# Kernel tuning notes

Measured on AMD Instinct MI355X. Metric: run time of the kernel, lower is better.

## Reference

```python
import jax, jax.numpy as jnp
import numpy as np

B, NA, DIN, H, DOUT = 8192, 32, 8, 64, 8  # B must be divisible by NA (final reshape)


def setup_inputs() -> dict:
    key = jax.random.key(0)
    ks = jax.random.split(key, 9)
    rn = lambda k, shp, s=1.0: jax.random.normal(k, shp, dtype=jnp.float32) * s
    return {
        "x": rn(ks[0], (B, NA, DIN)),
        "laplacian": jax.random.uniform(ks[1], (B, NA, 1), dtype=jnp.float32),
        "W_in": rn(ks[2], (H, DIN), 1.0 / np.sqrt(DIN)),
        "b_in": rn(ks[3], (H,), 0.01),
        "Aq": rn(ks[4], (H, H)),   # torch.randn init in original
        "Ak": rn(ks[5], (H, H)),
        "Av": rn(ks[6], (H, H)),
        "W_out": rn(ks[7], (DOUT, H), 1.0 / np.sqrt(H)),
        "b_out": rn(ks[8], (DOUT,), 0.01),
    }


def reference(x, laplacian, W_in, b_in, Aq, Ak, Av, W_out, b_out):
    silu = jax.nn.silu
    # mlp_in = SiLU(Linear); kron(laplacian, ones(1,1,H)) == broadcast of (B,na,1) mask
    h = silu(x @ W_in.T + b_in) * laplacian            # (B, na, H)
    # Q/K/V: weight @ h^T with swish; attention is over the HIDDEN axis (H x H scores)
    Q = silu(jnp.einsum('ij,bnj->bin', Aq, h))         # (B, H, na)
    K = silu(jnp.einsum('ij,bnj->bni', Ak, h))         # (B, na, H)
    V = silu(jnp.einsum('ij,bnj->bin', Av, h))         # (B, H, na)
    A = jax.nn.softmax(jnp.einsum('bin,bnj->bij', Q, K), axis=2)  # (B, H, H), softmax dim=2
    attn = silu(jnp.einsum('bij,bjn->bni', A, V))      # (B, na, H)
    # mlp_out = SiLU(Linear), masked again, mean over nodes, reshape (B/na, na, O)
    y = silu(attn @ W_out.T + b_out) * laplacian       # (B, na, O)
    return y.mean(axis=1).reshape(-1, NA, DOUT)        # (B/NA, NA, O)
```

## Files before the change

### kernel.cpp

```cpp
#include <hip/hip_runtime.h>

#define NB   8192
#define NA   32
#define DIN  8
#define HID  64
#define DOUT 8

typedef float     v4f __attribute__((ext_vector_type(4)));
typedef _Float16  v4h __attribute__((ext_vector_type(4)));

__device__ __forceinline__ float silu_f(float x) {
    return __fdividef(x, 1.0f + __expf(-x));
}

__device__ __forceinline__ v4h cvt4(v4f a) {
    v4h r;
    r[0] = (_Float16)a[0]; r[1] = (_Float16)a[1];
    r[2] = (_Float16)a[2]; r[3] = (_Float16)a[3];
    return r;
}

__device__ __forceinline__ v4h silu_cvt4(v4f a) {
    v4f s;
    s[0] = silu_f(a[0]); s[1] = silu_f(a[1]);
    s[2] = silu_f(a[2]); s[3] = silu_f(a[3]);
    return cvt4(s);
}

#define MFMA16(A, B, C) __builtin_amdgcn_mfma_f32_16x16x16f16((A), (B), (C), 0, 0, 0)

__global__ __launch_bounds__(256, 5) void attn_mfma_kernel(
    const float* __restrict__ x,
    const float* __restrict__ lap,
    const float* __restrict__ W_in,
    const float* __restrict__ b_in,
    const float* __restrict__ Aq,
    const float* __restrict__ Ak,
    const float* __restrict__ Av,
    const float* __restrict__ W_out,
    const float* __restrict__ b_out,
    float* __restrict__ out)
{
    __shared__ _Float16 wlds[3][16][64][4];
    __shared__ _Float16 hlds[4][4][64][4];

    const int t  = threadIdx.x;
    const int l  = t & 63;
    const int w  = t >> 6;
    const int lm = l & 15;
    const int lg = l >> 4;

    {
        const float* mats[3] = {Aq, Ak, Av};
        #pragma unroll
        for (int m = 0; m < 3; ++m) {
            #pragma unroll
            for (int f = 0; f < 4; ++f) {
                const int fid = w * 4 + f;
                const int it = fid >> 2, ks = fid & 3;
                v4f v = *(const v4f*)(mats[m] + (lm + 16 * it) * 64 + 16 * ks + 4 * lg);
                *(v4h*)&wlds[m][fid][l][0] = cvt4(v);
            }
        }
    }

    v4h zh = {};
    v4f zf = {};
    v4h winf[4];
    #pragma unroll
    for (int jt = 0; jt < 4; ++jt)
        winf[jt] = (lg < 2) ? cvt4(*(const v4f*)(W_in + (lm + 16 * jt) * 8 + 4 * lg)) : zh;
    v4h woutf[4];
    #pragma unroll
    for (int ks = 0; ks < 4; ++ks)
        woutf[ks] = (lm < 8) ? cvt4(*(const v4f*)(W_out + lm * 64 + 16 * ks + 4 * lg)) : zh;
    float binf[4];
    #pragma unroll
    for (int jt = 0; jt < 4; ++jt) binf[jt] = b_in[lm + 16 * jt];
    const float boutf = (lm < 8) ? b_out[lm] : 0.0f;

    __syncthreads();

    const int b = blockIdx.x * 4 + w;

    v4f lapv[2];
    lapv[0] = *(const v4f*)(lap + b * 32 + 4 * lg);
    lapv[1] = *(const v4f*)(lap + b * 32 + 16 + 4 * lg);

    v4h xf[2];
    #pragma unroll
    for (int nt = 0; nt < 2; ++nt)
        xf[nt] = (lg < 2) ? cvt4(*(const v4f*)(x + b * 256 + (lm + 16 * nt) * 8 + 4 * lg)) : zh;

    const int pr = l ^ lg;
    v4h hf[2][4];
    #pragma unroll
    for (int nt = 0; nt < 2; ++nt) {
        #pragma unroll
        for (int jt = 0; jt < 4; ++jt) {
            v4f hc = MFMA16(xf[nt], winf[jt], zf);
            #pragma unroll
            for (int r = 0; r < 4; ++r) {
                float hv = silu_f(hc[r] + binf[jt]) * lapv[nt][r];
                const int lr   = (4 * lg + r) | ((lm >> 2) << 4);
                const int phys = lr ^ (lm >> 2);
                hlds[w][jt][phys][lm & 3] = (_Float16)hv;
            }
        }
        __builtin_amdgcn_s_waitcnt(0);
        #pragma unroll
        for (int ks = 0; ks < 4; ++ks)
            hf[nt][ks] = *(v4h*)&hlds[w][ks][pr][0];
        __builtin_amdgcn_s_waitcnt(0);
    }

    v4h qf[2][4];
    {
        v4f acc[2][4] = {};
        #pragma unroll
        for (int it = 0; it < 4; ++it)
            #pragma unroll
            for (int ks = 0; ks < 4; ++ks) {
                v4h bw = *(v4h*)&wlds[0][it * 4 + ks][l][0];
                #pragma unroll
                for (int nt = 0; nt < 2; ++nt)
                    acc[nt][it] = MFMA16(hf[nt][ks], bw, acc[nt][it]);
            }
        #pragma unroll
        for (int nt = 0; nt < 2; ++nt)
            #pragma unroll
            for (int it = 0; it < 4; ++it) qf[nt][it] = silu_cvt4(acc[nt][it]);
    }
    v4h kf[2][4];
    {
        v4f acc[2][4] = {};
        #pragma unroll
        for (int it = 0; it < 4; ++it)
            #pragma unroll
            for (int ks = 0; ks < 4; ++ks) {
                v4h bw = *(v4h*)&wlds[1][it * 4 + ks][l][0];
                #pragma unroll
                for (int nt = 0; nt < 2; ++nt)
                    acc[nt][it] = MFMA16(hf[nt][ks], bw, acc[nt][it]);
            }
        #pragma unroll
        for (int nt = 0; nt < 2; ++nt)
            #pragma unroll
            for (int it = 0; it < 4; ++it) kf[nt][it] = silu_cvt4(acc[nt][it]);
    }
    v4h vf[4][2];
    {
        v4f acc[4][2] = {};
        #pragma unroll
        for (int it = 0; it < 4; ++it)
            #pragma unroll
            for (int ks = 0; ks < 4; ++ks) {
                v4h aw = *(v4h*)&wlds[2][it * 4 + ks][l][0];
                #pragma unroll
                for (int nt = 0; nt < 2; ++nt)
                    acc[it][nt] = MFMA16(aw, hf[nt][ks], acc[it][nt]);
            }
        #pragma unroll
        for (int it = 0; it < 4; ++it)
            #pragma unroll
            for (int nt = 0; nt < 2; ++nt) vf[it][nt] = silu_cvt4(acc[it][nt]);
    }

    v4f st[4][4] = {};
    #pragma unroll
    for (int jt = 0; jt < 4; ++jt)
        #pragma unroll
        for (int it = 0; it < 4; ++it)
            #pragma unroll
            for (int ns = 0; ns < 2; ++ns)
                st[jt][it] = MFMA16(kf[ns][jt], qf[ns][it], st[jt][it]);

    v4h pf[4][4];
    #pragma unroll
    for (int it = 0; it < 4; ++it) {
        float mx = st[0][it][0];
        #pragma unroll
        for (int jt = 0; jt < 4; ++jt)
            #pragma unroll
            for (int r = 0; r < 4; ++r) mx = fmaxf(mx, st[jt][it][r]);
        mx = fmaxf(mx, __shfl_xor(mx, 16, 64));
        mx = fmaxf(mx, __shfl_xor(mx, 32, 64));
        float sum = 0.0f;
        #pragma unroll
        for (int jt = 0; jt < 4; ++jt)
            #pragma unroll
            for (int r = 0; r < 4; ++r) {
                float e = __expf(st[jt][it][r] - mx);
                st[jt][it][r] = e;
                sum += e;
            }
        sum += __shfl_xor(sum, 16, 64);
        sum += __shfl_xor(sum, 32, 64);
        const float inv = __fdividef(1.0f, sum);
        #pragma unroll
        for (int jt = 0; jt < 4; ++jt) {
            v4f p = st[jt][it] * inv;
            pf[it][jt] = cvt4(p);
        }
    }

    v4f pv[4][2] = {};
    #pragma unroll
    for (int it = 0; it < 4; ++it)
        #pragma unroll
        for (int js = 0; js < 4; ++js)
            #pragma unroll
            for (int nt = 0; nt < 2; ++nt)
                pv[it][nt] = MFMA16(pf[it][js], vf[js][nt], pv[it][nt]);

    v4f ya[2] = {};
    #pragma unroll
    for (int nt = 0; nt < 2; ++nt)
        #pragma unroll
        for (int is = 0; is < 4; ++is)
            ya[nt] = MFMA16(silu_cvt4(pv[is][nt]), woutf[is], ya[nt]);

    float acc = 0.0f;
    #pragma unroll
    for (int nt = 0; nt < 2; ++nt)
        #pragma unroll
        for (int r = 0; r < 4; ++r)
            acc += silu_f(ya[nt][r] + boutf) * lapv[nt][r];
    acc += __shfl_xor(acc, 16, 64);
    acc += __shfl_xor(acc, 32, 64);
    if (l < 8) out[b * DOUT + l] = acc * (1.0f / NA);
}

extern "C" void kernel_launch(void* const* d_in, const int* in_sizes, int n_in,
                              void* d_out, int out_size, void* d_ws, size_t ws_size,
                              hipStream_t stream) {
    const float* x     = (const float*)d_in[0];
    const float* lap   = (const float*)d_in[1];
    const float* W_in  = (const float*)d_in[2];
    const float* b_in  = (const float*)d_in[3];
    const float* Aq    = (const float*)d_in[4];
    const float* Ak    = (const float*)d_in[5];
    const float* Av    = (const float*)d_in[6];
    const float* W_out = (const float*)d_in[7];
    const float* b_out = (const float*)d_in[8];
    attn_mfma_kernel<<<2048, 256, 0, stream>>>(x, lap, W_in, b_in, Aq, Ak, Av,
                                               W_out, b_out, (float*)d_out);
}
```

Baseline: 65.38 us.

## Fuse scores, softmax, PV and output projection per row tile; relax launch bounds

Restructures the attention pipeline so each 16-row tile of scores is computed, softmaxed, multiplied with V and projected through W_out before the next tile starts. This replaces the full 4x4 score and probability arrays held in registers. Q/K/V projections now accumulate one node tile at a time with weights reloaded from LDS per use, which lowers live accumulator count. Launch bounds go from 5 to 4 waves per SIMD, giving the compiler more registers but lowering the occupancy target. Reloading weight fragments doubles LDS reads, and the serialized per-tile chain may expose more MFMA latency.

Result: faster. 62.21 us (-4.8%).

```diff
diff --git a/kernel.cpp b/kernel.cpp
--- a/kernel.cpp
+++ b/kernel.cpp
@@ -29,7 +29,7 @@
 
 #define MFMA16(A, B, C) __builtin_amdgcn_mfma_f32_16x16x16f16((A), (B), (C), 0, 0, 0)
 
-__global__ __launch_bounds__(256, 5) void attn_mfma_kernel(
+__global__ __launch_bounds__(256, 4) void attn_mfma_kernel(
     const float* __restrict__ x,
     const float* __restrict__ lap,
     const float* __restrict__ W_in,
@@ -115,74 +115,57 @@
     }
 
     v4h qf[2][4];
-    {
-        v4f acc[2][4] = {};
+    #pragma unroll
+    for (int nt = 0; nt < 2; ++nt) {
+        v4f acc[4] = {};
         #pragma unroll
         for (int it = 0; it < 4; ++it)
             #pragma unroll
-            for (int ks = 0; ks < 4; ++ks) {
-                v4h bw = *(v4h*)&wlds[0][it * 4 + ks][l][0];
-                #pragma unroll
-                for (int nt = 0; nt < 2; ++nt)
-                    acc[nt][it] = MFMA16(hf[nt][ks], bw, acc[nt][it]);
-            }
-        #pragma unroll
-        for (int nt = 0; nt < 2; ++nt)
-            #pragma unroll
-            for (int it = 0; it < 4; ++it) qf[nt][it] = silu_cvt4(acc[nt][it]);
+            for (int ks = 0; ks < 4; ++ks)
+                acc[it] = MFMA16(hf[nt][ks], *(v4h*)&wlds[0][it * 4 + ks][l][0], acc[it]);
+        #pragma unroll
+        for (int it = 0; it < 4; ++it) qf[nt][it] = silu_cvt4(acc[it]);
     }
     v4h kf[2][4];
-    {
-        v4f acc[2][4] = {};
+    #pragma unroll
+    for (int nt = 0; nt < 2; ++nt) {
+        v4f acc[4] = {};
         #pragma unroll
         for (int it = 0; it < 4; ++it)
             #pragma unroll
-            for (int ks = 0; ks < 4; ++ks) {
-                v4h bw = *(v4h*)&wlds[1][it * 4 + ks][l][0];
-                #pragma unroll
-                for (int nt = 0; nt < 2; ++nt)
-                    acc[nt][it] = MFMA16(hf[nt][ks], bw, acc[nt][it]);
-            }
-        #pragma unroll
-        for (int nt = 0; nt < 2; ++nt)
-            #pragma unroll
-            for (int it = 0; it < 4; ++it) kf[nt][it] = silu_cvt4(acc[nt][it]);
+            for (int ks = 0; ks < 4; ++ks)
+                acc[it] = MFMA16(hf[nt][ks], *(v4h*)&wlds[1][it * 4 + ks][l][0], acc[it]);
+        #pragma unroll
+        for (int it = 0; it < 4; ++it) kf[nt][it] = silu_cvt4(acc[it]);
     }
     v4h vf[4][2];
-    {
-        v4f acc[4][2] = {};
+    #pragma unroll
+    for (int nt = 0; nt < 2; ++nt) {
+        v4f acc[4] = {};
         #pragma unroll
         for (int it = 0; it < 4; ++it)
             #pragma unroll
-            for (int ks = 0; ks < 4; ++ks) {
-                v4h aw = *(v4h*)&wlds[2][it * 4 + ks][l][0];
-                #pragma unroll
-                for (int nt = 0; nt < 2; ++nt)
-                    acc[it][nt] = MFMA16(aw, hf[nt][ks], acc[it][nt]);
-            }
-        #pragma unroll
-        for (int it = 0; it < 4; ++it)
-            #pragma unroll
-            for (int nt = 0; nt < 2; ++nt) vf[it][nt] = silu_cvt4(acc[it][nt]);
-    }
-
-    v4f st[4][4] = {};
-    #pragma unroll
-    for (int jt = 0; jt < 4; ++jt)
-        #pragma unroll
-        for (int it = 0; it < 4; ++it)
+            for (int ks = 0; ks < 4; ++ks)
+                acc[it] = MFMA16(*(v4h*)&wlds[2][it * 4 + ks][l][0], hf[nt][ks], acc[it]);
+        #pragma unroll
+        for (int it = 0; it < 4; ++it) vf[it][nt] = silu_cvt4(acc[it]);
+    }
+
+    v4f ya[2] = {};
+    #pragma unroll
+    for (int it = 0; it < 4; ++it) {
+        v4f s[4] = {};
+        #pragma unroll
+        for (int jt = 0; jt < 4; ++jt)
             #pragma unroll
             for (int ns = 0; ns < 2; ++ns)
-                st[jt][it] = MFMA16(kf[ns][jt], qf[ns][it], st[jt][it]);
-
-    v4h pf[4][4];
-    #pragma unroll
-    for (int it = 0; it < 4; ++it) {
-        float mx = st[0][it][0];
+                s[jt] = MFMA16(kf[ns][jt], qf[ns][it], s[jt]);
+
+        float mx = s[0][0];
         #pragma unroll
         for (int jt = 0; jt < 4; ++jt)
             #pragma unroll
-            for (int r = 0; r < 4; ++r) mx = fmaxf(mx, st[jt][it][r]);
+            for (int r = 0; r < 4; ++r) mx = fmaxf(mx, s[jt][r]);
         mx = fmaxf(mx, __shfl_xor(mx, 16, 64));
         mx = fmaxf(mx, __shfl_xor(mx, 32, 64));
         float sum = 0.0f;
@@ -190,35 +173,28 @@
         for (int jt = 0; jt < 4; ++jt)
             #pragma unroll
             for (int r = 0; r < 4; ++r) {
-                float e = __expf(st[jt][it][r] - mx);
-                st[jt][it][r] = e;
+                float e = __expf(s[jt][r] - mx);
+                s[jt][r] = e;
                 sum += e;
             }
         sum += __shfl_xor(sum, 16, 64);
         sum += __shfl_xor(sum, 32, 64);
         const float inv = __fdividef(1.0f, sum);
-        #pragma unroll
-        for (int jt = 0; jt < 4; ++jt) {
-            v4f p = st[jt][it] * inv;
-            pf[it][jt] = cvt4(p);
-        }
-    }
-
-    v4f pv[4][2] = {};
-    #pragma unroll
-    for (int it = 0; it < 4; ++it)
+        v4h pf[4];
+        #pragma unroll
+        for (int jt = 0; jt < 4; ++jt) pf[jt] = cvt4(s[jt] * inv);
+
+        v4f pv[2] = {};
         #pragma unroll
         for (int js = 0; js < 4; ++js)
             #pragma unroll
             for (int nt = 0; nt < 2; ++nt)
-                pv[it][nt] = MFMA16(pf[it][js], vf[js][nt], pv[it][nt]);
-
-    v4f ya[2] = {};
-    #pragma unroll
-    for (int nt = 0; nt < 2; ++nt)
-        #pragma unroll
-        for (int is = 0; is < 4; ++is)
-            ya[nt] = MFMA16(silu_cvt4(pv[is][nt]), woutf[is], ya[nt]);
+                pv[nt] = MFMA16(pf[js], vf[js][nt], pv[nt]);
+
+        #pragma unroll
+        for (int nt = 0; nt < 2; ++nt)
+            ya[nt] = MFMA16(silu_cvt4(pv[nt]), woutf[it], ya[nt]);
+    }
 
     float acc = 0.0f;
     #pragma unroll
```

## Fuse softmax and output projection per row tile, use 512-thread blocks

Applied to the files above, without the earlier changes.

The attention stage now handles one query row tile at a time: it computes scores, softmax, P·V, and that tile's share of the output projection inside a single loop. This avoids keeping the full 4x4 score tile array and the pv array live, which lowers register pressure. Blocks grow to 8 waves (512 threads), so the shared Aq/Ak/Av staging is spread across more waves and the weights are loaded into LDS half as often per batch row. The risk is that launch_bounds(512,4) may cap registers per thread and cause spills, and the per-tile loop leaves less MFMA work in flight to overlap with the exp/shuffle softmax.

Result: faster. 60.21 us (-7.9%).

```diff
diff --git a/kernel.cpp b/kernel.cpp
--- a/kernel.cpp
+++ b/kernel.cpp
@@ -29,7 +29,7 @@
 
 #define MFMA16(A, B, C) __builtin_amdgcn_mfma_f32_16x16x16f16((A), (B), (C), 0, 0, 0)
 
-__global__ __launch_bounds__(256, 5) void attn_mfma_kernel(
+__global__ __launch_bounds__(512, 4) void attn_mfma_kernel(
     const float* __restrict__ x,
     const float* __restrict__ lap,
     const float* __restrict__ W_in,
@@ -42,7 +42,7 @@
     float* __restrict__ out)
 {
     __shared__ _Float16 wlds[3][16][64][4];
-    __shared__ _Float16 hlds[4][4][64][4];
+    __shared__ _Float16 hlds[8][4][64][4];
 
     const int t  = threadIdx.x;
     const int l  = t & 63;
@@ -55,8 +55,8 @@
         #pragma unroll
         for (int m = 0; m < 3; ++m) {
             #pragma unroll
-            for (int f = 0; f < 4; ++f) {
-                const int fid = w * 4 + f;
+            for (int f = 0; f < 2; ++f) {
+                const int fid = w * 2 + f;
                 const int it = fid >> 2, ks = fid & 3;
                 v4f v = *(const v4f*)(mats[m] + (lm + 16 * it) * 64 + 16 * ks + 4 * lg);
                 *(v4h*)&wlds[m][fid][l][0] = cvt4(v);
@@ -81,7 +81,7 @@
 
     __syncthreads();
 
-    const int b = blockIdx.x * 4 + w;
+    const int b = blockIdx.x * 8 + w;
 
     v4f lapv[2];
     lapv[0] = *(const v4f*)(lap + b * 32 + 4 * lg);
@@ -166,23 +166,21 @@
             for (int nt = 0; nt < 2; ++nt) vf[it][nt] = silu_cvt4(acc[it][nt]);
     }
 
-    v4f st[4][4] = {};
-    #pragma unroll
-    for (int jt = 0; jt < 4; ++jt)
-        #pragma unroll
-        for (int it = 0; it < 4; ++it)
+    v4f ya[2] = {};
+    #pragma unroll
+    for (int it = 0; it < 4; ++it) {
+        v4f s[4] = {};
+        #pragma unroll
+        for (int jt = 0; jt < 4; ++jt)
             #pragma unroll
             for (int ns = 0; ns < 2; ++ns)
-                st[jt][it] = MFMA16(kf[ns][jt], qf[ns][it], st[jt][it]);
-
-    v4h pf[4][4];
-    #pragma unroll
-    for (int it = 0; it < 4; ++it) {
-        float mx = st[0][it][0];
+                s[jt] = MFMA16(kf[ns][jt], qf[ns][it], s[jt]);
+
+        float mx = s[0][0];
         #pragma unroll
         for (int jt = 0; jt < 4; ++jt)
             #pragma unroll
-            for (int r = 0; r < 4; ++r) mx = fmaxf(mx, st[jt][it][r]);
+            for (int r = 0; r < 4; ++r) mx = fmaxf(mx, s[jt][r]);
         mx = fmaxf(mx, __shfl_xor(mx, 16, 64));
         mx = fmaxf(mx, __shfl_xor(mx, 32, 64));
         float sum = 0.0f;
@@ -190,35 +188,28 @@
         for (int jt = 0; jt < 4; ++jt)
             #pragma unroll
             for (int r = 0; r < 4; ++r) {
-                float e = __expf(st[jt][it][r] - mx);
-                st[jt][it][r] = e;
+                float e = __expf(s[jt][r] - mx);
+                s[jt][r] = e;
                 sum += e;
             }
         sum += __shfl_xor(sum, 16, 64);
         sum += __shfl_xor(sum, 32, 64);
         const float inv = __fdividef(1.0f, sum);
-        #pragma unroll
-        for (int jt = 0; jt < 4; ++jt) {
-            v4f p = st[jt][it] * inv;
-            pf[it][jt] = cvt4(p);
-        }
-    }
-
-    v4f pv[4][2] = {};
-    #pragma unroll
-    for (int it = 0; it < 4; ++it)
+        v4h pf[4];
+        #pragma unroll
+        for (int jt = 0; jt < 4; ++jt) pf[jt] = cvt4(s[jt] * inv);
+
+        v4f pv[2] = {};
         #pragma unroll
         for (int js = 0; js < 4; ++js)
             #pragma unroll
             for (int nt = 0; nt < 2; ++nt)
-                pv[it][nt] = MFMA16(pf[it][js], vf[js][nt], pv[it][nt]);
-
-    v4f ya[2] = {};
-    #pragma unroll
-    for (int nt = 0; nt < 2; ++nt)
-        #pragma unroll
-        for (int is = 0; is < 4; ++is)
-            ya[nt] = MFMA16(silu_cvt4(pv[is][nt]), woutf[is], ya[nt]);
+                pv[nt] = MFMA16(pf[js], vf[js][nt], pv[nt]);
+
+        #pragma unroll
+        for (int nt = 0; nt < 2; ++nt)
+            ya[nt] = MFMA16(silu_cvt4(pv[nt]), woutf[it], ya[nt]);
+    }
 
     float acc = 0.0f;
     #pragma unroll
@@ -243,6 +234,6 @@
     const float* Av    = (const float*)d_in[6];
     const float* W_out = (const float*)d_in[7];
     const float* b_out = (const float*)d_in[8];
-    attn_mfma_kernel<<<2048, 256, 0, stream>>>(x, lap, W_in, b_in, Aq, Ak, Av,
+    attn_mfma_kernel<<<1024, 512, 0, stream>>>(x, lap, W_in, b_in, Aq, Ak, Av,
                                                W_out, b_out, (float*)d_out);
 }
```
